# Kernel optimization log

Measured on AMD Instinct MI355X. Metric: run time of the kernel, lower is better.

The kernel has to match this reference:

```python
import jax, jax.numpy as jnp
import numpy as np

B, L, D, H = 4, 1024, 768, 12
DH = D // H  # 64


def setup_inputs() -> dict:
    key = jax.random.key(0)
    kx, kk, kq, kv = jax.random.split(key, 4)
    # Original uses torch.rand (uniform [0,1)); scale by 1/D so pre-softmax
    # logits stay in a numerically sane range (same math, better conditioning).
    scale = 1.0 / D
    x = jax.random.normal(kx, (B, L, D), dtype=jnp.float32)
    k = jax.random.uniform(kk, (H, D, D), dtype=jnp.float32) * scale
    q = jax.random.uniform(kq, (H, D, D), dtype=jnp.float32) * scale
    v = jax.random.uniform(kv, (H, DH, D), dtype=jnp.float32) * scale
    return {"x": x, "k": k, "q": q, "v": v}


def reference(x, k, q, v):
    # x: [B, L, D]; torch permutes to [B, D, L] then 'bdl,ncd->bncl';
    # equivalent directly: 'bld,ncd->bncl'.
    K = jnp.einsum('bld,ncd->bncl', x, k)   # [B, H, D, L]
    Q = jnp.einsum('bld,ncd->bncl', x, q)   # [B, H, D, L]
    V = jnp.einsum('bld,ncd->bncl', x, v)   # [B, H, DH, L]
    scores = jnp.einsum('bndl,bndm->bnlm', Q, K)        # [B, H, L, L]
    S = jax.nn.softmax(scores, axis=-1)                  # softmax over dim 3
    R = jnp.einsum('bnkl,bndl->bndk', S, V)              # [B, H, DH, L]
    R = R.reshape(x.shape[0], D, -1)                     # [B, D, L]
    return jnp.transpose(R, (0, 2, 1))                   # [B, L, D]
```

## Files before the change

### kernel.cpp

```cpp
#include <hip/hip_runtime.h>
#include <hip/hip_bf16.h>
#include <stdint.h>
#include <stddef.h>

typedef unsigned short u16;
typedef __attribute__((ext_vector_type(8))) short short8;
typedef __attribute__((ext_vector_type(4))) float f32x4;
typedef __attribute__((ext_vector_type(16))) float f32x16;

#define NB 4
#define NL 1024
#define ND 768
#define NH 12
#define NDH 64

__device__ __forceinline__ u16 f2bf(float f) {
  __hip_bfloat16 h = __float2bfloat16(f);
  return *reinterpret_cast<u16*>(&h);
}
__device__ __forceinline__ float bf2f(u16 u) {
  __hip_bfloat16 h;
  *reinterpret_cast<u16*>(&h) = u;
  return __bfloat162float(h);
}

__device__ __forceinline__ void load16_to_lds(const u16* g, u16* l) {
  __builtin_amdgcn_global_load_lds(
      (__attribute__((address_space(1))) void*)(uintptr_t)g,
      (__attribute__((address_space(3))) void*)(uint32_t)(uintptr_t)l,
      16, 0, 0);
}

__global__ __launch_bounds__(256) void prep_inputs_kernel(
    const float* __restrict__ qI, const float* __restrict__ kI,
    u16* __restrict__ qT, u16* __restrict__ kTp,
    const float* __restrict__ x, u16* __restrict__ xb, int n4A,
    const float* __restrict__ vI, u16* __restrict__ vb, int n4B) {
  __shared__ float tile[32][33];
  int hz = blockIdx.z;
  if (hz == 2 * NH) {
    int i = (blockIdx.x + 24 * blockIdx.y) * 256 + threadIdx.x;
    int stride = 576 * 256;
    int tot = n4A + n4B;
    for (; i < tot; i += stride) {
      const float4* src;
      ushort4* dst;
      int j;
      if (i < n4A) { src = (const float4*)x; dst = (ushort4*)xb; j = i; }
      else         { src = (const float4*)vI; dst = (ushort4*)vb; j = i - n4A; }
      float4 f = src[j];
      ushort4 o;
      o.x = f2bf(f.x); o.y = f2bf(f.y); o.z = f2bf(f.z); o.w = f2bf(f.w);
      dst[j] = o;
    }
    return;
  }
  int h = (hz < NH) ? hz : hz - NH;
  const float* src = ((hz < NH) ? qI : kI) + (size_t)h * ND * ND;
  u16* dst = ((hz < NH) ? qT : kTp) + (size_t)h * ND * ND;
  int c0 = blockIdx.x * 32, r0 = blockIdx.y * 32;
  int tx = threadIdx.x & 31, ty = threadIdx.x >> 5;
#pragma unroll
  for (int i = 0; i < 32; i += 8)
    tile[ty + i][tx] = src[(size_t)(r0 + ty + i) * ND + c0 + tx];
  __syncthreads();
  int p = tx & 15, j = (tx >> 4) * 8 + ty;
#pragma unroll
  for (int i = 0; i < 32; i += 16) {
    ushort2 o;
    o.x = f2bf(tile[2 * p][j + i]);
    o.y = f2bf(tile[2 * p + 1][j + i]);
    *(ushort2*)&dst[(size_t)(c0 + j + i) * ND + r0 + 2 * p] = o;
  }
}

template <bool BF16_OUT, int IM, int IN, int KDIM, int LDC>
__global__ __launch_bounds__(256, 4) void gemm_bt(
    const u16* __restrict__ A, const u16* __restrict__ Bm, void* __restrict__ Cv,
    long sAb, long sAn, long sAz,
    long sBb, long sBn, long sBz,
    long sCb, long sCn, long sCz,
    int p0) {
  constexpr int BK = 64;
  constexpr int MTILE = IM * 64;
  constexpr int NTILE = IN * 64;
  constexpr int CPR = BK / 8;
  constexpr int ACH = MTILE * CPR / 256;
  constexpr int BCH = NTILE * CPR / 256;
  __shared__ __align__(16) u16 As[MTILE * BK];
  __shared__ __align__(16) u16 Bs[NTILE * BK];

  int id = blockIdx.x + gridDim.x * (blockIdx.y + gridDim.y * blockIdx.z);
  int total = gridDim.x * gridDim.y * gridDim.z;
  int xx, yy, zz;
  if ((total & 7) == 0) {
    int per = total >> 3;
    int wk = (id & 7) * per + (id >> 3);
    xx = wk % gridDim.x;
    int g2 = wk / gridDim.x;
    yy = g2 % gridDim.y;
    zz = g2 / gridDim.y;
  } else {
    xx = blockIdx.x; yy = blockIdx.y; zz = blockIdx.z;
  }

  int g = p0 + zz;
  int b = g / NH, n = g % NH;
  A  += (size_t)b * sAb + (size_t)n * sAn + (size_t)zz * sAz;
  Bm += (size_t)b * sBb + (size_t)n * sBn + (size_t)zz * sBz;
  size_t cOff = (size_t)b * sCb + (size_t)n * sCn + (size_t)zz * sCz;

  int m0 = yy * MTILE, n0 = xx * NTILE;
  int t = threadIdx.x;
  int lane = t & 63, w = t >> 6;
  int m32 = lane & 31, kg = lane >> 5;
  int wm = w >> 1, wn = w & 1;

  const u16* gAb;
  const u16* gBb;
  {
    int r = t / CPR;
    int cc = (t & (CPR - 1)) ^ (r & 7);
    gAb = A + (size_t)(m0 + r) * KDIM + cc * 8;
    gBb = Bm + (size_t)(n0 + r) * KDIM + cc * 8;
  }

  f32x16 acc[IM][IN];
#pragma unroll
  for (int i = 0; i < IM; i++)
#pragma unroll
    for (int j = 0; j < IN; j++)
#pragma unroll
      for (int r = 0; r < 16; r++) acc[i][j][r] = 0.f;

#pragma unroll 1
  for (int k0 = 0; k0 < KDIM; k0 += BK) {
    __syncthreads();
#pragma unroll
    for (int u = 0; u < ACH; u++)
      load16_to_lds(gAb + (size_t)u * 32 * KDIM, &As[(size_t)(u * 256 + w * 64) * 8]);
    gAb += BK;
#pragma unroll
    for (int u = 0; u < BCH; u++)
      load16_to_lds(gBb + (size_t)u * 32 * KDIM, &Bs[(size_t)(u * 256 + w * 64) * 8]);
    gBb += BK;
    __syncthreads();

#pragma unroll
    for (int kc = 0; kc < 2; kc++) {
      short8 af[IM][2], bfr[IN][2];
#pragma unroll
      for (int i = 0; i < IM; i++) {
        int row = wm * (IM * 32) + i * 32 + m32;
#pragma unroll
        for (int h = 0; h < 2; h++) {
          int ck = (kc * 4 + h * 2 + kg) ^ (row & 7);
          af[i][h] = *(const short8*)&As[row * BK + ck * 8];
        }
      }
#pragma unroll
      for (int j = 0; j < IN; j++) {
        int row = wn * (IN * 32) + j * 32 + m32;
#pragma unroll
        for (int h = 0; h < 2; h++) {
          int ck = (kc * 4 + h * 2 + kg) ^ (row & 7);
          bfr[j][h] = *(const short8*)&Bs[row * BK + ck * 8];
        }
      }
#pragma unroll
      for (int i = 0; i < IM; i++)
#pragma unroll
        for (int j = 0; j < IN; j++) {
          acc[i][j] = __builtin_amdgcn_mfma_f32_32x32x16_bf16(af[i][0], bfr[j][0], acc[i][j], 0, 0, 0);
          acc[i][j] = __builtin_amdgcn_mfma_f32_32x32x16_bf16(af[i][1], bfr[j][1], acc[i][j], 0, 0, 0);
        }
    }
  }

#pragma unroll
  for (int i = 0; i < IM; i++) {
#pragma unroll
    for (int j = 0; j < IN; j++) {
      int colg = n0 + wn * (IN * 32) + j * 32 + m32;
#pragma unroll
      for (int r = 0; r < 16; r++) {
        int rowg = m0 + wm * (IM * 32) + i * 32 + (r & 3) + 8 * (r >> 2) + 4 * kg;
        float vv = acc[i][j][r];
        if (BF16_OUT) {
          ((u16*)Cv)[cOff + (size_t)rowg * LDC + colg] = f2bf(vv);
        } else {
          ((float*)Cv)[cOff + (size_t)rowg * LDC + colg] = vv;
        }
      }
    }
  }
}

__global__ __launch_bounds__(256, 4) void gemm_prep(
    const u16* __restrict__ kT, const u16* __restrict__ qT, u16* __restrict__ MTp,
    const u16* __restrict__ vb, const u16* __restrict__ xb, u16* __restrict__ V2p) {
  constexpr int BK = 64;
  constexpr int KDIM = ND;
  constexpr int CPR = BK / 8;
  constexpr long DD = (long)ND * ND;
  constexpr long LD = (long)NL * ND;
  __shared__ __align__(16) u16 As[128 * BK];
  __shared__ __align__(16) u16 Bs[128 * BK];

  int id = blockIdx.x + gridDim.x * (blockIdx.y + gridDim.y * blockIdx.z);
  int total = gridDim.x * gridDim.y * gridDim.z;
  int per = total >> 3;
  int wk = (id & 7) * per + (id >> 3);
  int xx = wk % gridDim.x;
  int g2 = wk / gridDim.x;
  int yy = g2 % gridDim.y;
  int zz = g2 / gridDim.y;

  const u16* A;
  const u16* Bm;
  u16* C;
  int ldc;
  if (zz < NH) {
    if (xx >= 6) return;
    A = kT + (size_t)zz * DD;
    Bm = qT + (size_t)zz * DD;
    C = MTp + (size_t)zz * DD;
    ldc = ND;
  } else {
    int b = zz - NH;
    A = vb;
    Bm = xb + (size_t)b * LD;
    C = V2p + (size_t)b * NH * NDH * NL;
    ldc = NL;
  }

  int m0 = yy * 128, n0 = xx * 128;
  int t = threadIdx.x;
  int lane = t & 63, w = t >> 6;
  int m32 = lane & 31, kg = lane >> 5;
  int wm = w >> 1, wn = w & 1;

  const u16* gAb;
  const u16* gBb;
  {
    int r = t / CPR;
    int cc = (t & (CPR - 1)) ^ (r & 7);
    gAb = A + (size_t)(m0 + r) * KDIM + cc * 8;
    gBb = Bm + (size_t)(n0 + r) * KDIM + cc * 8;
  }

  f32x16 acc[2][2];
#pragma unroll
  for (int i = 0; i < 2; i++)
#pragma unroll
    for (int j = 0; j < 2; j++)
#pragma unroll
      for (int r = 0; r < 16; r++) acc[i][j][r] = 0.f;

#pragma unroll 1
  for (int k0 = 0; k0 < KDIM; k0 += BK) {
    __syncthreads();
#pragma unroll
    for (int u = 0; u < 4; u++)
      load16_to_lds(gAb + (size_t)u * 32 * KDIM, &As[(size_t)(u * 256 + w * 64) * 8]);
    gAb += BK;
#pragma unroll
    for (int u = 0; u < 4; u++)
      load16_to_lds(gBb + (size_t)u * 32 * KDIM, &Bs[(size_t)(u * 256 + w * 64) * 8]);
    gBb += BK;
    __syncthreads();

#pragma unroll
    for (int kc = 0; kc < 2; kc++) {
      short8 af[2][2], bfr[2][2];
#pragma unroll
      for (int i = 0; i < 2; i++) {
        int row = wm * 64 + i * 32 + m32;
#pragma unroll
        for (int h = 0; h < 2; h++) {
          int ck = (kc * 4 + h * 2 + kg) ^ (row & 7);
          af[i][h] = *(const short8*)&As[row * BK + ck * 8];
        }
      }
#pragma unroll
      for (int j = 0; j < 2; j++) {
        int row = wn * 64 + j * 32 + m32;
#pragma unroll
        for (int h = 0; h < 2; h++) {
          int ck = (kc * 4 + h * 2 + kg) ^ (row & 7);
          bfr[j][h] = *(const short8*)&Bs[row * BK + ck * 8];
        }
      }
#pragma unroll
      for (int i = 0; i < 2; i++)
#pragma unroll
        for (int j = 0; j < 2; j++) {
          acc[i][j] = __builtin_amdgcn_mfma_f32_32x32x16_bf16(af[i][0], bfr[j][0], acc[i][j], 0, 0, 0);
          acc[i][j] = __builtin_amdgcn_mfma_f32_32x32x16_bf16(af[i][1], bfr[j][1], acc[i][j], 0, 0, 0);
        }
    }
  }

#pragma unroll
  for (int i = 0; i < 2; i++) {
#pragma unroll
    for (int j = 0; j < 2; j++) {
      int colg = n0 + wn * 64 + j * 32 + m32;
#pragma unroll
      for (int r = 0; r < 16; r++) {
        int rowg = m0 + wm * 64 + i * 32 + (r & 3) + 8 * (r >> 2) + 4 * kg;
        C[(size_t)rowg * ldc + colg] = f2bf(acc[i][j][r]);
      }
    }
  }
}

template <int OUTMODE, int KDIM, int LDC>
__global__ __launch_bounds__(512, 2) void gemm256_8p(
    const u16* __restrict__ A, const u16* __restrict__ Bm, void* __restrict__ Cv,
    long sAb, long sAn, long sAz,
    long sBb, long sBn, long sBz,
    long sCb, long sCn, long sCz,
    int p0) {
  constexpr int BK = 64;
  constexpr int NT = KDIM / BK;
  constexpr int NC = NT / 2;
  static_assert(KDIM % 128 == 0 && NC >= 2, "need even #K-tiles and >=2 cycles");
  __shared__ __align__(16) u16 As[2][256 * BK];
  __shared__ __align__(16) u16 Bs[2][256 * BK];

  int id = blockIdx.x + gridDim.x * (blockIdx.y + gridDim.y * blockIdx.z);
  int total = gridDim.x * gridDim.y * gridDim.z;
  int xx, yy, zz;
  if ((total & 7) == 0) {
    int per = total >> 3;
    int wk = (id & 7) * per + (id >> 3);
    xx = wk % gridDim.x;
    int g2 = wk / gridDim.x;
    yy = g2 % gridDim.y;
    zz = g2 / gridDim.y;
  } else {
    xx = blockIdx.x; yy = blockIdx.y; zz = blockIdx.z;
  }

  int g = p0 + zz;
  int b = g / NH, n = g % NH;
  A  += (size_t)b * sAb + (size_t)n * sAn + (size_t)zz * sAz;
  Bm += (size_t)b * sBb + (size_t)n * sBn + (size_t)zz * sBz;
  size_t cOff = (size_t)b * sCb + (size_t)n * sCn + (size_t)zz * sCz;

  int m0 = yy * 256, n0 = xx * 256;
  int t = threadIdx.x;
  int lane = t & 63, w = t >> 6;
  int wm = w >> 2, wn = w & 3;
  int l15 = lane & 15, q4 = lane >> 4;

  int r0 = t >> 3;
  int cc0 = (t & 7) ^ (r0 & 7);
  const u16* gA = A + (size_t)(m0 + r0) * KDIM + cc0 * 8;
  const u16* gB = Bm + (size_t)(n0 + r0) * KDIM + cc0 * 8;
  int wslab = w * 512;

#define STG_A1(d, h, u, kt) load16_to_lds( \
    gA + (size_t)((h) * 128 + (u) * 64) * KDIM + (size_t)(kt) * BK, \
    &As[d][((h) * 128 + (u) * 64) * BK + wslab])
#define STG_B1(d, h, u, kt) load16_to_lds( \
    gB + (size_t)((h) * 128 + (u) * 64) * KDIM + (size_t)(kt) * BK, \
    &Bs[d][((h) * 128 + (u) * 64) * BK + wslab])
#define STG_A2(d, h, kt) do { STG_A1(d, h, 0, kt); STG_A1(d, h, 1, kt); } while (0)
#define STG_B2(d, h, kt) do { STG_B1(d, h, 0, kt); STG_B1(d, h, 1, kt); } while (0)

#define READ_A(d, qm, dst) do { \
  _Pragma("unroll") for (int fm = 0; fm < 4; fm++) { \
    int row = (qm) * 128 + wm * 64 + fm * 16 + l15; \
    _Pragma("unroll") for (int ks = 0; ks < 2; ks++) { \
      int ck = (ks * 4 + q4) ^ (row & 7); \
      dst[fm][ks] = *(const short8*)&As[d][row * BK + ck * 8]; \
    } \
  } \
} while (0)

#define READ_B(d, qn, dst) do { \
  _Pragma("unroll") for (int fn = 0; fn < 2; fn++) { \
    int row = (qn) * 128 + wn * 32 + fn * 16 + l15; \
    _Pragma("unroll") for (int ks = 0; ks < 2; ks++) { \
      int ck = (ks * 4 + q4) ^ (row & 7); \
      dst[fn][ks] = *(const short8*)&Bs[d][row * BK + ck * 8]; \
    } \
  } \
} while (0)

#define MF_Q(qm, qn, AR, BR) do { \
  __builtin_amdgcn_s_setprio(1); \
  _Pragma("unroll") for (int ks = 0; ks < 2; ks++) \
    _Pragma("unroll") for (int fm = 0; fm < 4; fm++) \
      _Pragma("unroll") for (int fn = 0; fn < 2; fn++) \
        acc[qm][qn][fm][fn] = __builtin_amdgcn_mfma_f32_16x16x32_bf16( \
            AR[fm][ks], BR[fn][ks], acc[qm][qn][fm][fn], 0, 0, 0); \
  __builtin_amdgcn_s_setprio(0); \
} while (0)

#define PH_SYNC() do { \
  __builtin_amdgcn_s_barrier(); \
  asm volatile("s_waitcnt lgkmcnt(0)" ::: "memory"); \
  __builtin_amdgcn_sched_barrier(0); \
} while (0)
#define PH_END() do { \
  __builtin_amdgcn_s_barrier(); \
  __builtin_amdgcn_sched_barrier(0); \
} while (0)

  f32x4 acc[2][2][4][2];
#pragma unroll
  for (int qm = 0; qm < 2; qm++)
#pragma unroll
    for (int qn = 0; qn < 2; qn++)
#pragma unroll
      for (int fm = 0; fm < 4; fm++)
#pragma unroll
        for (int fn = 0; fn < 2; fn++)
          acc[qm][qn][fm][fn] = (f32x4){0.f, 0.f, 0.f, 0.f};

  STG_A2(0, 0, 0); STG_A2(0, 1, 0);
  STG_B2(0, 0, 0); STG_B2(0, 1, 0);
  STG_A2(1, 0, 1); STG_A2(1, 1, 1);
  STG_B2(1, 0, 1); STG_B2(1, 1, 1);
  asm volatile("s_waitcnt vmcnt(8)" ::: "memory");
  __builtin_amdgcn_s_barrier();
  __builtin_amdgcn_sched_barrier(0);

#pragma unroll 1
  for (int cyc = 0; cyc < NC; ++cyc) {
    int t0 = cyc * 2;
    bool full = (cyc + 1 < NC);
    short8 af0[4][2], af1[4][2], bq0[2][2], bq1[2][2];

    READ_A(0, 0, af0); READ_B(0, 0, bq0);
    PH_SYNC(); MF_Q(0, 0, af0, bq0); PH_END();
    READ_B(0, 1, bq1);
    if (full) { STG_A2(0, 0, t0 + 2); STG_B2(0, 0, t0 + 2); }
    PH_SYNC(); MF_Q(0, 1, af0, bq1); PH_END();
    READ_A(0, 1, af1);
    if (full) STG_B2(0, 1, t0 + 2);
    PH_SYNC(); MF_Q(1, 0, af1, bq0); PH_END();
    if (full) STG_A2(0, 1, t0 + 2);
    __builtin_amdgcn_s_barrier();
    MF_Q(1, 1, af1, bq1);
    __builtin_amdgcn_sched_barrier(0);
    if (full) asm volatile("s_waitcnt vmcnt(8)" ::: "memory");
    else      asm volatile("s_waitcnt vmcnt(0)" ::: "memory");
    PH_END();

    READ_A(1, 0, af0); READ_B(1, 0, bq0);
    PH_SYNC(); MF_Q(0, 0, af0, bq0); PH_END();
    READ_B(1, 1, bq1);
    if (full) { STG_A2(1, 0, t0 + 3); STG_B2(1, 0, t0 + 3); }
    PH_SYNC(); MF_Q(0, 1, af0, bq1); PH_END();
    READ_A(1, 1, af1);
    if (full) STG_B2(1, 1, t0 + 3);
    PH_SYNC(); MF_Q(1, 0, af1, bq0); PH_END();
    if (full) {
      STG_A2(1, 1, t0 + 3);
      __builtin_amdgcn_s_barrier();
      MF_Q(1, 1, af1, bq1);
      __builtin_amdgcn_sched_barrier(0);
      asm volatile("s_waitcnt vmcnt(8)" ::: "memory");
      PH_END();
    } else {
      __builtin_amdgcn_s_barrier();
      MF_Q(1, 1, af1, bq1);
    }
  }

#pragma unroll
  for (int qm = 0; qm < 2; qm++)
#pragma unroll
    for (int qn = 0; qn < 2; qn++)
#pragma unroll
      for (int fm = 0; fm < 4; fm++)
#pragma unroll
        for (int fn = 0; fn < 2; fn++) {
          int colg = n0 + qn * 128 + wn * 32 + fn * 16 + l15;
#pragma unroll
          for (int r = 0; r < 4; r++) {
            int rowg = m0 + qm * 128 + wm * 64 + fm * 16 + q4 * 4 + r;
            float vv = acc[qm][qn][fm][fn][r];
            if (OUTMODE == 2) vv = __expf(vv);
            if (OUTMODE >= 1) {
              ((u16*)Cv)[cOff + (size_t)rowg * LDC + colg] = f2bf(vv);
            } else {
              ((float*)Cv)[cOff + (size_t)rowg * LDC + colg] = vv;
            }
          }
        }
#undef STG_A1
#undef STG_B1
#undef STG_A2
#undef STG_B2
#undef READ_A
#undef READ_B
#undef MF_Q
#undef PH_SYNC
#undef PH_END
}

__global__ __launch_bounds__(256) void softmax_pv_kernel(
    const u16* __restrict__ Pb, const u16* __restrict__ V2, float* __restrict__ out,
    int p0) {
  __shared__ __align__(16) u16 Ps[64 * 128];
  __shared__ __align__(16) u16 Vs[64 * 128];

  int id = blockIdx.x + gridDim.x * blockIdx.y;
  int total = gridDim.x * gridDim.y;
  int xx, zz;
  if ((total & 7) == 0) {
    int per = total >> 3;
    int wk = (id & 7) * per + (id >> 3);
    xx = wk & 15; zz = wk >> 4;
  } else {
    xx = blockIdx.x; zz = blockIdx.y;
  }

  int g = p0 + zz;
  int b = g / NH, n = g % NH;
  const u16* S = Pb + (size_t)zz * NL * NL;
  const u16* V = V2 + (size_t)g * NDH * NL;

  int l0 = xx * 64;
  int t = threadIdx.x;
  int lane = t & 63, w = t >> 6;
  int row16 = lane & 15, q = lane >> 4;
  int rs = row16 & 7;

  f32x4 acc[5];
#pragma unroll
  for (int j = 0; j < 5; j++) acc[j] = (f32x4){0.f, 0.f, 0.f, 0.f};

  short8 onesf;
  {
    short val = (row16 == 0) ? (short)0x3F80 : (short)0;
#pragma unroll
    for (int e = 0; e < 8; e++) onesf[e] = val;
  }

  const u16* ssrc[4];
  const u16* vsrc[4];
#pragma unroll
  for (int u = 0; u < 4; u++) {
    int c = u * 256 + t;
    int r = c >> 4, cc = (c & 15) ^ (r & 7);
    ssrc[u] = S + (size_t)(l0 + r) * NL + cc * 8;
    vsrc[u] = V + (size_t)r * NL + cc * 8;
  }

#pragma unroll 1
  for (int mt = 0; mt < 8; mt++) {
    int mo = mt * 128;
    __syncthreads();
#pragma unroll
    for (int u = 0; u < 4; u++)
      load16_to_lds(ssrc[u] + mo, &Ps[(size_t)(u * 256 + w * 64) * 8]);
#pragma unroll
    for (int u = 0; u < 4; u++)
      load16_to_lds(vsrc[u] + mo, &Vs[(size_t)(u * 256 + w * 64) * 8]);
    __syncthreads();

#pragma unroll
    for (int kk = 0; kk < 4; kk++) {
      int ch = ((kk * 4 + q) ^ rs) * 16;
      int lrow = w * 16 + row16;
      short8 paf = *(const short8*)((const char*)Ps + lrow * 256 + ch);
      short8 bfr[4];
#pragma unroll
      for (int j = 0; j < 4; j++) {
        int dh = j * 16 + row16;
        bfr[j] = *(const short8*)((const char*)Vs + dh * 256 + ch);
      }
#pragma unroll
      for (int j = 0; j < 4; j++)
        acc[j] = __builtin_amdgcn_mfma_f32_16x16x32_bf16(paf, bfr[j], acc[j], 0, 0, 0);
      acc[4] = __builtin_amdgcn_mfma_f32_16x16x32_bf16(paf, onesf, acc[4], 0, 0, 0);
    }
  }

#pragma unroll
  for (int r = 0; r < 4; r++) {
    float sum = __shfl(acc[4][r], lane & 48, 64);
    float inv = 1.0f / sum;
    int row = l0 + w * 16 + q * 4 + r;
    float* op = out + ((size_t)b * NL + row) * ND + n * NDH;
#pragma unroll
    for (int j = 0; j < 4; j++)
      op[j * 16 + row16] = acc[j][r] * inv;
  }
}

extern "C" void kernel_launch(void* const* d_in, const int* in_sizes, int n_in,
                              void* d_out, int out_size, void* d_ws, size_t ws_size,
                              hipStream_t stream) {
  (void)in_sizes; (void)n_in; (void)out_size;
  const float* x  = (const float*)d_in[0];
  const float* kI = (const float*)d_in[1];
  const float* qI = (const float*)d_in[2];
  const float* vI = (const float*)d_in[3];
  float* out = (float*)d_out;

  size_t off = 0;
  char* wsb = (char*)d_ws;
  auto alloc = [&](size_t bytes) -> char* {
    char* p = wsb + off;
    off += (bytes + 255) & ~(size_t)255;
    return p;
  };
  u16* xb = (u16*)alloc((size_t)NB * NL * ND * 2);
  u16* vb = (u16*)alloc((size_t)NH * NDH * ND * 2);
  u16* MT = (u16*)alloc((size_t)NH * ND * ND * 2);
  u16* V2 = (u16*)alloc((size_t)NB * NH * NDH * NL * 2);
  size_t fixedSz = off;

  u16* qT = (u16*)alloc((size_t)NH * ND * ND * 2);
  u16* kT = (u16*)alloc((size_t)NH * ND * ND * 2);
  size_t scratchEndQK = off;

  const size_t Tsz  = (size_t)NL * ND * 2;
  const size_t Ssz  = (size_t)NL * NL * 2;
  const size_t perPair = Tsz + Ssz;

  int chunk = NB * NH;
  {
    size_t avail = ws_size > fixedSz ? ws_size - fixedSz : 0;
    size_t maxChunk = avail / perPair;
    if (maxChunk < 1) maxChunk = 1;
    if (maxChunk < (size_t)chunk) {
      int passes = (int)(((size_t)NB * NH + maxChunk - 1) / maxChunk);
      chunk = (NB * NH + passes - 1) / passes;
    }
  }
  off = fixedSz;
  u16* T  = (u16*)alloc((size_t)chunk * Tsz);
  u16* Sb = (u16*)alloc((size_t)chunk * Ssz);
  if (off < scratchEndQK) off = scratchEndQK;

  const long DD  = (long)ND * ND;
  const long LD  = (long)NL * ND;
  const long LL  = (long)NL * NL;

  {
    int n4A = NB * NL * ND / 4;
    int n4B = NH * NDH * ND / 4;
    prep_inputs_kernel<<<dim3(24, 24, 2 * NH + 1), dim3(256), 0, stream>>>(
        qI, kI, qT, kT, x, xb, n4A, vI, vb, n4B);
  }

  gemm_prep<<<dim3(8, 6, 16), dim3(256), 0, stream>>>(kT, qT, MT, vb, xb, V2);

  for (int p0 = 0; p0 < NB * NH; p0 += chunk) {
    int c = NB * NH - p0;
    if (c > chunk) c = chunk;
    gemm_bt<true, 2, 2, 768, ND><<<dim3(6, 8, c), dim3(256), 0, stream>>>(
        xb, MT, T,
        LD, 0, 0,  0, DD, 0,  0, 0, LD, p0);
    gemm256_8p<2, 768, NL><<<dim3(4, 4, c), dim3(512), 0, stream>>>(
        T, xb, Sb,
        0, 0, LD,  LD, 0, 0,  0, 0, LL, p0);
    softmax_pv_kernel<<<dim3(16, c), dim3(256), 0, stream>>>(Sb, V2, out, p0);
  }
}
```

Baseline: 297.4 us.

## Move V projection GEMM from prep launch into first T-GEMM launch

The V2 projection (v times x) is moved out of the gemm_prep launch, which now computes only the 12 MT = kT·qT products on a 6x6x12 grid with no early-exit blocks. The V2 work is appended as extra z-slices to the first chunk's T = x·MT GEMM launch through a new combined gemm_TV2 kernel. The aim is to even out per-launch load: gemm_prep no longer wastes idle blocks, and the T GEMM's grid gets more blocks to fill the GPU. This adds per-block branching, and V2 must be complete before softmax_pv, which still holds because it runs in the first chunk.

```diff
diff --git a/kernel.cpp b/kernel.cpp
--- a/kernel.cpp
+++ b/kernel.cpp
@@ -74,136 +74,12 @@
   }
 }
 
-template <bool BF16_OUT, int IM, int IN, int KDIM, int LDC>
-__global__ __launch_bounds__(256, 4) void gemm_bt(
-    const u16* __restrict__ A, const u16* __restrict__ Bm, void* __restrict__ Cv,
-    long sAb, long sAn, long sAz,
-    long sBb, long sBn, long sBz,
-    long sCb, long sCn, long sCz,
-    int p0) {
-  constexpr int BK = 64;
-  constexpr int MTILE = IM * 64;
-  constexpr int NTILE = IN * 64;
-  constexpr int CPR = BK / 8;
-  constexpr int ACH = MTILE * CPR / 256;
-  constexpr int BCH = NTILE * CPR / 256;
-  __shared__ __align__(16) u16 As[MTILE * BK];
-  __shared__ __align__(16) u16 Bs[NTILE * BK];
-
-  int id = blockIdx.x + gridDim.x * (blockIdx.y + gridDim.y * blockIdx.z);
-  int total = gridDim.x * gridDim.y * gridDim.z;
-  int xx, yy, zz;
-  if ((total & 7) == 0) {
-    int per = total >> 3;
-    int wk = (id & 7) * per + (id >> 3);
-    xx = wk % gridDim.x;
-    int g2 = wk / gridDim.x;
-    yy = g2 % gridDim.y;
-    zz = g2 / gridDim.y;
-  } else {
-    xx = blockIdx.x; yy = blockIdx.y; zz = blockIdx.z;
-  }
-
-  int g = p0 + zz;
-  int b = g / NH, n = g % NH;
-  A  += (size_t)b * sAb + (size_t)n * sAn + (size_t)zz * sAz;
-  Bm += (size_t)b * sBb + (size_t)n * sBn + (size_t)zz * sBz;
-  size_t cOff = (size_t)b * sCb + (size_t)n * sCn + (size_t)zz * sCz;
-
-  int m0 = yy * MTILE, n0 = xx * NTILE;
-  int t = threadIdx.x;
-  int lane = t & 63, w = t >> 6;
-  int m32 = lane & 31, kg = lane >> 5;
-  int wm = w >> 1, wn = w & 1;
-
-  const u16* gAb;
-  const u16* gBb;
-  {
-    int r = t / CPR;
-    int cc = (t & (CPR - 1)) ^ (r & 7);
-    gAb = A + (size_t)(m0 + r) * KDIM + cc * 8;
-    gBb = Bm + (size_t)(n0 + r) * KDIM + cc * 8;
-  }
-
-  f32x16 acc[IM][IN];
-#pragma unroll
-  for (int i = 0; i < IM; i++)
-#pragma unroll
-    for (int j = 0; j < IN; j++)
-#pragma unroll
-      for (int r = 0; r < 16; r++) acc[i][j][r] = 0.f;
-
-#pragma unroll 1
-  for (int k0 = 0; k0 < KDIM; k0 += BK) {
-    __syncthreads();
-#pragma unroll
-    for (int u = 0; u < ACH; u++)
-      load16_to_lds(gAb + (size_t)u * 32 * KDIM, &As[(size_t)(u * 256 + w * 64) * 8]);
-    gAb += BK;
-#pragma unroll
-    for (int u = 0; u < BCH; u++)
-      load16_to_lds(gBb + (size_t)u * 32 * KDIM, &Bs[(size_t)(u * 256 + w * 64) * 8]);
-    gBb += BK;
-    __syncthreads();
-
-#pragma unroll
-    for (int kc = 0; kc < 2; kc++) {
-      short8 af[IM][2], bfr[IN][2];
-#pragma unroll
-      for (int i = 0; i < IM; i++) {
-        int row = wm * (IM * 32) + i * 32 + m32;
-#pragma unroll
-        for (int h = 0; h < 2; h++) {
-          int ck = (kc * 4 + h * 2 + kg) ^ (row & 7);
-          af[i][h] = *(const short8*)&As[row * BK + ck * 8];
-        }
-      }
-#pragma unroll
-      for (int j = 0; j < IN; j++) {
-        int row = wn * (IN * 32) + j * 32 + m32;
-#pragma unroll
-        for (int h = 0; h < 2; h++) {
-          int ck = (kc * 4 + h * 2 + kg) ^ (row & 7);
-          bfr[j][h] = *(const short8*)&Bs[row * BK + ck * 8];
-        }
-      }
-#pragma unroll
-      for (int i = 0; i < IM; i++)
-#pragma unroll
-        for (int j = 0; j < IN; j++) {
-          acc[i][j] = __builtin_amdgcn_mfma_f32_32x32x16_bf16(af[i][0], bfr[j][0], acc[i][j], 0, 0, 0);
-          acc[i][j] = __builtin_amdgcn_mfma_f32_32x32x16_bf16(af[i][1], bfr[j][1], acc[i][j], 0, 0, 0);
-        }
-    }
-  }
-
-#pragma unroll
-  for (int i = 0; i < IM; i++) {
-#pragma unroll
-    for (int j = 0; j < IN; j++) {
-      int colg = n0 + wn * (IN * 32) + j * 32 + m32;
-#pragma unroll
-      for (int r = 0; r < 16; r++) {
-        int rowg = m0 + wm * (IM * 32) + i * 32 + (r & 3) + 8 * (r >> 2) + 4 * kg;
-        float vv = acc[i][j][r];
-        if (BF16_OUT) {
-          ((u16*)Cv)[cOff + (size_t)rowg * LDC + colg] = f2bf(vv);
-        } else {
-          ((float*)Cv)[cOff + (size_t)rowg * LDC + colg] = vv;
-        }
-      }
-    }
-  }
-}
-
 __global__ __launch_bounds__(256, 4) void gemm_prep(
-    const u16* __restrict__ kT, const u16* __restrict__ qT, u16* __restrict__ MTp,
-    const u16* __restrict__ vb, const u16* __restrict__ xb, u16* __restrict__ V2p) {
+    const u16* __restrict__ kT, const u16* __restrict__ qT, u16* __restrict__ MTp) {
   constexpr int BK = 64;
   constexpr int KDIM = ND;
   constexpr int CPR = BK / 8;
   constexpr long DD = (long)ND * ND;
-  constexpr long LD = (long)NL * ND;
   __shared__ __align__(16) u16 As[128 * BK];
   __shared__ __align__(16) u16 Bs[128 * BK];
 
@@ -216,25 +92,134 @@
   int yy = g2 % gridDim.y;
   int zz = g2 / gridDim.y;
 
+  const u16* A = kT + (size_t)zz * DD;
+  const u16* Bm = qT + (size_t)zz * DD;
+  u16* C = MTp + (size_t)zz * DD;
+
+  int m0 = yy * 128, n0 = xx * 128;
+  int t = threadIdx.x;
+  int lane = t & 63, w = t >> 6;
+  int m32 = lane & 31, kg = lane >> 5;
+  int wm = w >> 1, wn = w & 1;
+
+  const u16* gAb;
+  const u16* gBb;
+  {
+    int r = t / CPR;
+    int cc = (t & (CPR - 1)) ^ (r & 7);
+    gAb = A + (size_t)(m0 + r) * KDIM + cc * 8;
+    gBb = Bm + (size_t)(n0 + r) * KDIM + cc * 8;
+  }
+
+  f32x16 acc[2][2];
+#pragma unroll
+  for (int i = 0; i < 2; i++)
+#pragma unroll
+    for (int j = 0; j < 2; j++)
+#pragma unroll
+      for (int r = 0; r < 16; r++) acc[i][j][r] = 0.f;
+
+#pragma unroll 1
+  for (int k0 = 0; k0 < KDIM; k0 += BK) {
+    __syncthreads();
+#pragma unroll
+    for (int u = 0; u < 4; u++)
+      load16_to_lds(gAb + (size_t)u * 32 * KDIM, &As[(size_t)(u * 256 + w * 64) * 8]);
+    gAb += BK;
+#pragma unroll
+    for (int u = 0; u < 4; u++)
+      load16_to_lds(gBb + (size_t)u * 32 * KDIM, &Bs[(size_t)(u * 256 + w * 64) * 8]);
+    gBb += BK;
+    __syncthreads();
+
+#pragma unroll
+    for (int kc = 0; kc < 2; kc++) {
+      short8 af[2][2], bfr[2][2];
+#pragma unroll
+      for (int i = 0; i < 2; i++) {
+        int row = wm * 64 + i * 32 + m32;
+#pragma unroll
+        for (int h = 0; h < 2; h++) {
+          int ck = (kc * 4 + h * 2 + kg) ^ (row & 7);
+          af[i][h] = *(const short8*)&As[row * BK + ck * 8];
+        }
+      }
+#pragma unroll
+      for (int j = 0; j < 2; j++) {
+        int row = wn * 64 + j * 32 + m32;
+#pragma unroll
+        for (int h = 0; h < 2; h++) {
+          int ck = (kc * 4 + h * 2 + kg) ^ (row & 7);
+          bfr[j][h] = *(const short8*)&Bs[row * BK + ck * 8];
+        }
+      }
+#pragma unroll
+      for (int i = 0; i < 2; i++)
+#pragma unroll
+        for (int j = 0; j < 2; j++) {
+          acc[i][j] = __builtin_amdgcn_mfma_f32_32x32x16_bf16(af[i][0], bfr[j][0], acc[i][j], 0, 0, 0);
+          acc[i][j] = __builtin_amdgcn_mfma_f32_32x32x16_bf16(af[i][1], bfr[j][1], acc[i][j], 0, 0, 0);
+        }
+    }
+  }
+
+#pragma unroll
+  for (int i = 0; i < 2; i++) {
+#pragma unroll
+    for (int j = 0; j < 2; j++) {
+      int colg = n0 + wn * 64 + j * 32 + m32;
+#pragma unroll
+      for (int r = 0; r < 16; r++) {
+        int rowg = m0 + wm * 64 + i * 32 + (r & 3) + 8 * (r >> 2) + 4 * kg;
+        C[(size_t)rowg * ND + colg] = f2bf(acc[i][j][r]);
+      }
+    }
+  }
+}
+
+__global__ __launch_bounds__(256, 4) void gemm_TV2(
+    const u16* __restrict__ xb, const u16* __restrict__ MTp, u16* __restrict__ Tout,
+    const u16* __restrict__ vb, u16* __restrict__ V2p, int p0, int cT) {
+  constexpr int BK = 64;
+  constexpr int KDIM = ND;
+  constexpr int CPR = BK / 8;
+  constexpr long DD = (long)ND * ND;
+  constexpr long LD = (long)NL * ND;
+  __shared__ __align__(16) u16 As[128 * BK];
+  __shared__ __align__(16) u16 Bs[128 * BK];
+
+  int id = blockIdx.x + gridDim.x * (blockIdx.y + gridDim.y * blockIdx.z);
+  int total = gridDim.x * gridDim.y * gridDim.z;
+  int per = total >> 3;
+  int wk = (id & 7) * per + (id >> 3);
+  int xx = wk % gridDim.x;
+  int g2 = wk / gridDim.x;
+  int yy = g2 % gridDim.y;
+  int zz = g2 / gridDim.y;
+
   const u16* A;
   const u16* Bm;
   u16* C;
-  int ldc;
-  if (zz < NH) {
-    if (xx >= 6) return;
-    A = kT + (size_t)zz * DD;
-    Bm = qT + (size_t)zz * DD;
-    C = MTp + (size_t)zz * DD;
+  int ldc, m0, n0;
+  if (zz < cT) {
+    int g = p0 + zz;
+    int b = g / NH, n = g % NH;
+    A = xb + (size_t)b * LD;
+    Bm = MTp + (size_t)n * DD;
+    C = Tout + (size_t)zz * LD;
     ldc = ND;
+    m0 = xx * 128;
+    n0 = yy * 128;
   } else {
-    int b = zz - NH;
+    int b = zz - cT;
     A = vb;
     Bm = xb + (size_t)b * LD;
     C = V2p + (size_t)b * NH * NDH * NL;
     ldc = NL;
-  }
-
-  int m0 = yy * 128, n0 = xx * 128;
+    m0 = yy * 128;
+    n0 = xx * 128;
+  }
+
   int t = threadIdx.x;
   int lane = t & 63, w = t >> 6;
   int m32 = lane & 31, kg = lane >> 5;
@@ -641,7 +626,6 @@
   u16* Sb = (u16*)alloc((size_t)chunk * Ssz);
   if (off < scratchEndQK) off = scratchEndQK;
 
-  const long DD  = (long)ND * ND;
   const long LD  = (long)NL * ND;
   const long LL  = (long)NL * NL;
 
@@ -652,14 +636,13 @@
         qI, kI, qT, kT, x, xb, n4A, vI, vb, n4B);
   }
 
-  gemm_prep<<<dim3(8, 6, 16), dim3(256), 0, stream>>>(kT, qT, MT, vb, xb, V2);
+  gemm_prep<<<dim3(6, 6, 12), dim3(256), 0, stream>>>(kT, qT, MT);
 
   for (int p0 = 0; p0 < NB * NH; p0 += chunk) {
     int c = NB * NH - p0;
     if (c > chunk) c = chunk;
-    gemm_bt<true, 2, 2, 768, ND><<<dim3(6, 8, c), dim3(256), 0, stream>>>(
-        xb, MT, T,
-        LD, 0, 0,  0, DD, 0,  0, 0, LD, p0);
+    int zT = c + ((p0 == 0) ? NB : 0);
+    gemm_TV2<<<dim3(8, 6, zT), dim3(256), 0, stream>>>(xb, MT, T, vb, V2, p0, c);
     gemm256_8p<2, 768, NL><<<dim3(4, 4, c), dim3(512), 0, stream>>>(
         T, xb, Sb,
         0, 0, LD,  LD, 0, 0,  0, 0, LL, p0);
```

New measurement: 297.6 us. About the same (+0.1%).
